# Optimization experiments

Measured on AMD Instinct MI355X. Metric: run time of the kernel, lower is better.

## Reference

```python
import jax, jax.numpy as jnp
import numpy as np

B, C, H, W = 8, 256, 64, 64
GROUPS = 8
EPS = 1e-5


def setup_inputs() -> dict:
    key = jax.random.key(0)
    ks = jax.random.split(key, 10)
    s = 1.0 / np.sqrt(C)
    return {
        "x": jax.random.normal(ks[0], (B, C, H, W), dtype=jnp.float32),
        "gn_gamma": jnp.ones((C,), jnp.float32),
        "gn_beta": jnp.zeros((C,), jnp.float32),
        "wq": jax.random.uniform(ks[1], (C, C), jnp.float32, -s, s),
        "bq": jax.random.uniform(ks[2], (C,), jnp.float32, -s, s),
        "wk": jax.random.uniform(ks[3], (C, C), jnp.float32, -s, s),
        "bk": jax.random.uniform(ks[4], (C,), jnp.float32, -s, s),
        "wv": jax.random.uniform(ks[5], (C, C), jnp.float32, -s, s),
        "bv": jax.random.uniform(ks[6], (C,), jnp.float32, -s, s),
        "wp": jax.random.uniform(ks[7], (C, C), jnp.float32, -s, s),
        "bp": jax.random.uniform(ks[8], (C,), jnp.float32, -s, s),
    }


def _group_norm(x, gamma, beta):
    b, c, h, w = x.shape
    xg = x.reshape(b, GROUPS, c // GROUPS, h, w)
    mu = jnp.mean(xg, axis=(2, 3, 4), keepdims=True)
    var = jnp.mean(jnp.square(xg - mu), axis=(2, 3, 4), keepdims=True)
    xn = ((xg - mu) * jax.lax.rsqrt(var + EPS)).reshape(b, c, h, w)
    return xn * gamma[None, :, None, None] + beta[None, :, None, None]


def reference(x, gn_gamma, gn_beta, wq, bq, wk, bk, wv, bv, wp, bp):
    b, c, h, w = x.shape
    xn = _group_norm(x, gn_gamma, gn_beta)
    xf = xn.reshape(b, c, h * w)  # [b, c, n]
    # 1x1 Conv1d == per-position channel matmul
    q = jnp.einsum('oc,bcn->bon', wq, xf) + bq[None, :, None]
    k = jnp.einsum('oc,bcn->bon', wk, xf) + bk[None, :, None]
    v = jnp.einsum('oc,bcn->bon', wv, xf) + bv[None, :, None]
    scale = 1.0 / jnp.sqrt(jnp.asarray(c, xf.dtype))
    # attn[b,i,j] = softmax_j(q[:,i]^T k[:,j] / sqrt(c))
    attn = jax.nn.softmax(jnp.einsum('bci,bcj->bij', q, k) * scale, axis=-1)
    # out[b,c,i] = sum_j v[b,c,j] * attn[b,i,j]
    out = jnp.einsum('bcj,bij->bci', v, attn)
    out = jnp.einsum('oc,bcn->bon', wp, out) + bp[None, :, None]
    return x + out.reshape(b, c, h, w)
```

## Files before the change

### kernel.cpp

```cpp
#include <hip/hip_runtime.h>


typedef __bf16 bf16x8 __attribute__((ext_vector_type(8)));
typedef __bf16 bf16x4 __attribute__((ext_vector_type(4)));
typedef float floatx4 __attribute__((ext_vector_type(4)));
typedef float floatx16 __attribute__((ext_vector_type(16)));

constexpr int Bb = 8, Cc_ = 256, HW = 4096;
constexpr int BNT = Bb * HW;

__device__ __forceinline__ void load_lds16(const void* g, void* l) {
  __builtin_amdgcn_global_load_lds((const __attribute__((address_space(1))) void*)g,
                                   (__attribute__((address_space(3))) void*)l, 16, 0, 0);
}

#define MEMFENCE asm volatile("" ::: "memory")
__device__ __forceinline__ void bar_sync() {
  MEMFENCE;
  __builtin_amdgcn_s_barrier();
  MEMFENCE;
}

__global__ __launch_bounds__(256) void gn_part(const float* __restrict__ x,
                                               float* __restrict__ part) {
  int sub = blockIdx.x & 7;
  int bg = blockIdx.x >> 3;
  const float4* p = (const float4*)(x + (size_t)bg * 131072 + (size_t)sub * 16384);
  int tid = threadIdx.x;
  float s = 0.f, ss = 0.f;
#pragma unroll
  for (int i = 0; i < 16; ++i) {
    float4 v = p[i * 256 + tid];
    s += v.x + v.y + v.z + v.w;
    ss += v.x * v.x + v.y * v.y + v.z * v.z + v.w * v.w;
  }
  for (int off = 32; off; off >>= 1) { s += __shfl_down(s, off); ss += __shfl_down(ss, off); }
  __shared__ float red[8];
  int wv = tid >> 6, ln = tid & 63;
  if (ln == 0) { red[wv] = s; red[4 + wv] = ss; }
  __syncthreads();
  if (tid == 0) {
    part[blockIdx.x * 2] = red[0] + red[1] + red[2] + red[3];
    part[blockIdx.x * 2 + 1] = red[4] + red[5] + red[6] + red[7];
  }
}

__global__ __launch_bounds__(256) void gn_norm_t(const float* __restrict__ x,
                                                 const float* __restrict__ part,
                                                 const float* __restrict__ gamma,
                                                 const float* __restrict__ beta,
                                                 __bf16* __restrict__ Xt) {
  __shared__ float tile[64][65];
  __shared__ float sst[4];
  int b = blockIdx.z, c0 = blockIdx.y * 64, n0 = blockIdx.x * 64;
  int tid = threadIdx.x;
  if (tid < 2) {
    int g = b * 8 + (c0 >> 5) + tid;
    float s = 0.f, ss = 0.f;
#pragma unroll
    for (int k = 0; k < 8; ++k) { s += part[(g * 8 + k) * 2]; ss += part[(g * 8 + k) * 2 + 1]; }
    float mean = s / 131072.f;
    float var = ss / 131072.f - mean * mean;
    sst[tid * 2] = mean;
    sst[tid * 2 + 1] = rsqrtf(var + 1e-5f);
  }
  int cl = tid >> 4, nl = (tid & 15) * 4;
  const float* xb = x + ((size_t)b * Cc_ + c0) * HW + n0;
#pragma unroll
  for (int i = 0; i < 4; ++i) {
    int c = cl + i * 16;
    float4 v = *(const float4*)&xb[(size_t)c * HW + nl];
    tile[c][nl] = v.x; tile[c][nl + 1] = v.y; tile[c][nl + 2] = v.z; tile[c][nl + 3] = v.w;
  }
  __syncthreads();
#pragma unroll
  for (int i = 0; i < 16; ++i) {
    int idx = i * 256 + tid;
    int n = idx >> 6, c = idx & 63;
    int gc = c0 + c;
    float mean = sst[(c >> 5) * 2], rstd = sst[(c >> 5) * 2 + 1];
    float v = (tile[c][n] - mean) * rstd * gamma[gc] + beta[gc];
    Xt[((size_t)b * HW + n0 + n) * Cc_ + gc] = (__bf16)v;
  }
}

__global__ __launch_bounds__(256) void pack_w(const float* __restrict__ wq, const float* __restrict__ wk,
                                              const float* __restrict__ wv, const float* __restrict__ wp,
                                              const float* __restrict__ bq, const float* __restrict__ bk,
                                              const float* __restrict__ bv, const float* __restrict__ bp,
                                              __bf16* __restrict__ Wqk, __bf16* __restrict__ Wv,
                                              __bf16* __restrict__ Wp, float* __restrict__ Bqk,
                                              float* __restrict__ Bv, float* __restrict__ Bp) {
  int i = blockIdx.x * 256 + threadIdx.x;
  if (i < 65536) {
    Wqk[i] = (__bf16)wq[i];
    Wqk[65536 + i] = (__bf16)wk[i];
    Wv[i] = (__bf16)wv[i];
    Wp[i] = (__bf16)wp[i];
  }
  if (i < 256) { Bqk[i] = bq[i]; Bqk[256 + i] = bk[i]; Bv[i] = bv[i]; Bp[i] = bp[i]; }
}

template <int BM, int BN, int WM, int WN, int EPI>
__global__ __launch_bounds__(256) void gemm_bt(
    const __bf16* __restrict__ A, int lda,
    const __bf16* __restrict__ B, int ldb,
    __bf16* __restrict__ C, int ldc,
    int K, float scale,
    const float* __restrict__ bias,
    const float* __restrict__ resid,
    float* __restrict__ outF) {
  constexpr int TM = WM / 16, TN = WN / 16;
  __shared__ __bf16 As[BM * 32];
  __shared__ __bf16 Bs[BN * 32];

  const int tid = threadIdx.x;
  const int wave = tid >> 6, lane = tid & 63;
  const int wr = wave >> 1, wc = wave & 1;
  const int quad = lane >> 4, l16 = lane & 15;
  const int m0 = blockIdx.y * BM, n0 = blockIdx.x * BN;
  const int srow = lane >> 2;
  const int scol = (lane & 3) * 8;

  floatx4 acc[TM][TN] = {};

  const int kTiles = K / 32;
  for (int kt = 0; kt < kTiles; ++kt) {
    const int k0 = kt * 32;
    __syncthreads();
#pragma unroll
    for (int i = 0; i < BM / 64; ++i) {
      int row = i * 64 + wave * 16 + srow;
      load_lds16(A + (size_t)(m0 + row) * lda + k0 + scol, &As[(i * 64 + wave * 16) * 32]);
    }
#pragma unroll
    for (int i = 0; i < BN / 64; ++i) {
      int row = i * 64 + wave * 16 + srow;
      load_lds16(B + (size_t)(n0 + row) * ldb + k0 + scol, &Bs[(i * 64 + wave * 16) * 32]);
    }
    __syncthreads();

    bf16x8 af[TM], bfr[TN];
#pragma unroll
    for (int i = 0; i < TM; ++i)
      af[i] = *(const bf16x8*)&As[(wr * WM + i * 16 + l16) * 32 + quad * 8];
#pragma unroll
    for (int j = 0; j < TN; ++j)
      bfr[j] = *(const bf16x8*)&Bs[(wc * WN + j * 16 + l16) * 32 + quad * 8];
#pragma unroll
    for (int i = 0; i < TM; ++i)
#pragma unroll
      for (int j = 0; j < TN; ++j)
        acc[i][j] = __builtin_amdgcn_mfma_f32_16x16x32_bf16(af[i], bfr[j], acc[i][j], 0, 0, 0);
  }

#pragma unroll
  for (int i = 0; i < TM; ++i) {
#pragma unroll
    for (int j = 0; j < TN; ++j) {
      int gc = n0 + wc * WN + j * 16 + l16;
#pragma unroll
      for (int r = 0; r < 4; ++r) {
        int gr = m0 + wr * WM + i * 16 + quad * 4 + r;
        float v = acc[i][j][r] * scale;
        if constexpr (EPI == 1) v += bias[gc];
        if constexpr (EPI == 2) v += bias[gr];
        if constexpr (EPI == 3) {
          int bb = gc >> 12, nn = gc & 4095;
          size_t oidx = (size_t)bb * (Cc_ * HW) + (size_t)gr * HW + nn;
          outF[oidx] = v + bias[gr] + resid[oidx];
        } else {
          C[(size_t)gr * ldc + gc] = (__bf16)v;
        }
      }
    }
  }
}

__global__ __launch_bounds__(256, 2) void flash_attn(const __bf16* __restrict__ QK,
                                                     const __bf16* __restrict__ V,
                                                     __bf16* __restrict__ O) {
  __shared__ __align__(16) __bf16 smem[36864];
  __shared__ float Lb[2][64];
  __shared__ __align__(16) float Linv[64];
  __bf16* Ks = smem;
  __bf16* Vt = smem + 16384;
  __bf16* Pb = smem + 32768;

  const int tid = threadIdx.x;
  const int w = tid >> 6, lane = tid & 63;
  const int r = w & 1, h = w >> 1;
  const int l31 = lane & 31, hh = lane >> 5;
  const int b = blockIdx.x & 7;
  const int m0 = (blockIdx.x >> 3) * 64;
  const int q = 32 * r + l31;

  bf16x8 qf[16];
  {
    const size_t qrow = (size_t)(b * HW + m0 + q);
#pragma unroll
    for (int kc = 0; kc < 16; ++kc) {
      qf[kc] = *(const bf16x8*)&QK[qrow * 512 + kc * 16 + hh * 8];
#pragma unroll
      for (int e = 0; e < 8; ++e) qf[kc][e] = (__bf16)((float)qf[kc][e] * 0.0625f);
    }
  }

  floatx16 oacc[4] = {};
  float l_run = 0.f;

  const int ks_slot = lane & 31, ks_rin = lane >> 5;
  const int vt_slot = lane & 7, vt_rin = lane >> 3;

#pragma unroll
  for (int i = 0; i < 8; ++i) {
    int rl = w * 16 + i * 2 + ks_rin;
    load_lds16(QK + (size_t)(b * HW + rl) * 512 + 256 + ((ks_slot ^ (rl & 31)) << 3),
               &Ks[(w * 16 + i * 2) * 256]);
  }

  for (int jt = 0; jt < 64; ++jt) {
    const int j0 = jt * 64;
    asm volatile("s_waitcnt lgkmcnt(0)" ::: "memory");
    bar_sync();
#pragma unroll
    for (int i = 0; i < 8; ++i) {
      int cl = w * 64 + i * 8 + vt_rin;
      load_lds16(V + (size_t)cl * BNT + (b * HW + j0 + ((vt_slot ^ (cl & 7)) << 3)),
                 &Vt[(w * 64 + i * 8) * 64]);
    }
    asm volatile("s_waitcnt vmcnt(8)" ::: "memory");
    bar_sync();

    floatx16 sacc = {};
    {
      const int jl = 32 * h + l31;
      const __bf16* krow = &Ks[jl * 256];
      const int jx = jl & 31;
      __builtin_amdgcn_s_setprio(1);
#pragma unroll
      for (int kc = 0; kc < 16; ++kc) {
        bf16x8 kfv = *(const bf16x8*)&krow[((kc * 2 + hh) ^ jx) << 3];
        sacc = __builtin_amdgcn_mfma_f32_32x32x16_bf16(kfv, qf[kc], sacc, 0, 0, 0);
      }
      __builtin_amdgcn_s_setprio(0);
    }

    float ls = 0.f;
#pragma unroll
    for (int i = 0; i < 16; ++i) {
      float p = __expf(sacc[i]);
      sacc[i] = p;
      ls += p;
    }
    l_run += ls;
#pragma unroll
    for (int g = 0; g < 4; ++g) {
      bf16x4 pk;
#pragma unroll
      for (int k = 0; k < 4; ++k) pk[k] = (__bf16)sacc[g * 4 + k];
      *(bf16x4*)&Pb[q * 64 + ((((4 * h + g) ^ (l31 & 7)) << 3) + 4 * hh)] = pk;
    }

    asm volatile("s_waitcnt vmcnt(0) lgkmcnt(0)" ::: "memory");
    bar_sync();

    if (jt < 63) {
#pragma unroll
      for (int i = 0; i < 8; ++i) {
        int rl = w * 16 + i * 2 + ks_rin;
        load_lds16(QK + (size_t)(b * HW + j0 + 64 + rl) * 512 + 256 + ((ks_slot ^ (rl & 31)) << 3),
                   &Ks[(w * 16 + i * 2) * 256]);
      }
    }

    __builtin_amdgcn_s_setprio(1);
#pragma unroll
    for (int ks = 0; ks < 4; ++ks) {
      bf16x8 pf = *(const bf16x8*)&Pb[q * 64 + (((ks * 2 + hh) ^ (l31 & 7)) << 3)];
#pragma unroll
      for (int nt = 0; nt < 4; ++nt) {
        int cl = h * 128 + nt * 32 + l31;
        bf16x8 vf = *(const bf16x8*)&Vt[cl * 64 + (((ks * 2 + hh) ^ (cl & 7)) << 3)];
        oacc[nt] = __builtin_amdgcn_mfma_f32_32x32x16_bf16(pf, vf, oacc[nt], 0, 0, 0);
      }
    }
    __builtin_amdgcn_s_setprio(0);
  }

  __syncthreads();
  float l2 = l_run + __shfl_xor(l_run, 32);
  if (hh == 0) Lb[h][q] = l2;
  __syncthreads();
  if (tid < 64) Linv[tid] = 1.f / (Lb[0][tid] + Lb[1][tid]);
  __syncthreads();
  __bf16* Os = smem;
#pragma unroll
  for (int g = 0; g < 4; ++g) {
    floatx4 lv = *(const floatx4*)&Linv[32 * r + g * 8 + 4 * hh];
#pragma unroll
    for (int k = 0; k < 4; ++k) {
      int qloc = 32 * r + g * 8 + 4 * hh + k;
#pragma unroll
      for (int nt = 0; nt < 4; ++nt) {
        int c = h * 128 + nt * 32 + l31;
        Os[qloc * 256 + c] = (__bf16)(oacc[nt][g * 4 + k] * lv[k]);
      }
    }
  }
  __syncthreads();
  const float4* src = (const float4*)Os;
  float4* dst = (float4*)(O + (size_t)(b * HW + m0) * 256);
#pragma unroll
  for (int i = 0; i < 8; ++i) dst[i * 256 + tid] = src[i * 256 + tid];
}

extern "C" void kernel_launch(void* const* d_in, const int* in_sizes, int n_in,
                              void* d_out, int out_size, void* d_ws, size_t ws_size,
                              hipStream_t stream) {
  const float* x = (const float*)d_in[0];
  const float* gamma = (const float*)d_in[1];
  const float* beta = (const float*)d_in[2];
  const float* wq = (const float*)d_in[3];
  const float* bq = (const float*)d_in[4];
  const float* wk = (const float*)d_in[5];
  const float* bk = (const float*)d_in[6];
  const float* wv = (const float*)d_in[7];
  const float* bv = (const float*)d_in[8];
  const float* wp = (const float*)d_in[9];
  const float* bp = (const float*)d_in[10];
  float* out = (float*)d_out;

  char* ws = (char*)d_ws;
  size_t off = 0;
  auto alloc = [&](size_t n) { size_t o = off; off = (off + n + 255) & ~(size_t)255; return o; };
  __bf16* XT = (__bf16*)(ws + alloc((size_t)BNT * Cc_ * 2));
  __bf16* QK = (__bf16*)(ws + alloc((size_t)BNT * 512 * 2));
  __bf16* V  = (__bf16*)(ws + alloc((size_t)Cc_ * BNT * 2));
  __bf16* O  = (__bf16*)(ws + alloc((size_t)BNT * Cc_ * 2));
  __bf16* WQK = (__bf16*)(ws + alloc(512 * 256 * 2));
  __bf16* WV  = (__bf16*)(ws + alloc(256 * 256 * 2));
  __bf16* WP  = (__bf16*)(ws + alloc(256 * 256 * 2));
  float* BQK = (float*)(ws + alloc(512 * 4));
  float* BV  = (float*)(ws + alloc(256 * 4));
  float* BP  = (float*)(ws + alloc(256 * 4));
  float* PART = (float*)(ws + alloc(512 * 2 * 4));

  pack_w<<<dim3(256), dim3(256), 0, stream>>>(wq, wk, wv, wp, bq, bk, bv, bp,
                                              WQK, WV, WP, BQK, BV, BP);
  gn_part<<<dim3(512), dim3(256), 0, stream>>>(x, PART);
  gn_norm_t<<<dim3(64, 4, 8), dim3(256), 0, stream>>>(x, PART, gamma, beta, XT);

  gemm_bt<128, 128, 64, 64, 1><<<dim3(512 / 128, BNT / 128), dim3(256), 0, stream>>>(
      XT, 256, WQK, 256, QK, 512, 256, 1.0f, BQK, nullptr, nullptr);
  gemm_bt<128, 128, 64, 64, 2><<<dim3(BNT / 128, 256 / 128), dim3(256), 0, stream>>>(
      WV, 256, XT, 256, V, BNT, 256, 1.0f, BV, nullptr, nullptr);

  flash_attn<<<dim3(512), dim3(256), 0, stream>>>(QK, V, O);

  gemm_bt<128, 128, 64, 64, 3><<<dim3(BNT / 128, 256 / 128), dim3(256), 0, stream>>>(
      WP, 256, O, 256, nullptr, 0, 256, 1.0f, BP, x, out);
}
```

Measured before the change: 317.8 us.

## Prefetch K tiles into registers and double-buffer V in LDS in flash attention

Flash attention now loads K tiles straight from global memory into per-wave registers and issues the load for the next tile right after the score MFMAs, instead of staging K through shared memory. V tiles are double-buffered in shared memory, and the next tile is fetched while the current one is consumed. This cuts the barriers per iteration from three to two and lets global loads overlap with compute. In exchange it uses about 64 more VGPRs per thread, and waves that share the same h re-fetch the same K rows from global or L2 rather than sharing one LDS copy.

```diff
diff --git a/kernel.cpp b/kernel.cpp
--- a/kernel.cpp
+++ b/kernel.cpp
@@ -183,8 +183,6 @@
   __shared__ __align__(16) __bf16 smem[36864];
   __shared__ float Lb[2][64];
   __shared__ __align__(16) float Linv[64];
-  __bf16* Ks = smem;
-  __bf16* Vt = smem + 16384;
   __bf16* Pb = smem + 32768;
 
   const int tid = threadIdx.x;
@@ -206,44 +204,38 @@
     }
   }
 
+  const __bf16* kbase = QK + (size_t)(b * HW + 32 * h + l31) * 512 + 256 + hh * 8;
+  bf16x8 kf[16];
+#pragma unroll
+  for (int kc = 0; kc < 16; ++kc) kf[kc] = *(const bf16x8*)&kbase[kc * 16];
+
+  const int vt_slot = lane & 7, vt_rin = lane >> 3;
+#pragma unroll
+  for (int i = 0; i < 8; ++i) {
+    int cl = w * 64 + i * 8 + vt_rin;
+    load_lds16(V + (size_t)cl * BNT + (b * HW + ((vt_slot ^ (cl & 7)) << 3)),
+               &smem[(w * 64 + i * 8) * 64]);
+  }
+
   floatx16 oacc[4] = {};
   float l_run = 0.f;
 
-  const int ks_slot = lane & 31, ks_rin = lane >> 5;
-  const int vt_slot = lane & 7, vt_rin = lane >> 3;
-
-#pragma unroll
-  for (int i = 0; i < 8; ++i) {
-    int rl = w * 16 + i * 2 + ks_rin;
-    load_lds16(QK + (size_t)(b * HW + rl) * 512 + 256 + ((ks_slot ^ (rl & 31)) << 3),
-               &Ks[(w * 16 + i * 2) * 256]);
-  }
-
   for (int jt = 0; jt < 64; ++jt) {
     const int j0 = jt * 64;
-    asm volatile("s_waitcnt lgkmcnt(0)" ::: "memory");
-    bar_sync();
-#pragma unroll
-    for (int i = 0; i < 8; ++i) {
-      int cl = w * 64 + i * 8 + vt_rin;
-      load_lds16(V + (size_t)cl * BNT + (b * HW + j0 + ((vt_slot ^ (cl & 7)) << 3)),
-                 &Vt[(w * 64 + i * 8) * 64]);
-    }
-    asm volatile("s_waitcnt vmcnt(8)" ::: "memory");
-    bar_sync();
+    __bf16* Vc = smem + ((jt & 1) << 14);
+    __bf16* Vn = smem + (((jt + 1) & 1) << 14);
 
     floatx16 sacc = {};
-    {
-      const int jl = 32 * h + l31;
-      const __bf16* krow = &Ks[jl * 256];
-      const int jx = jl & 31;
-      __builtin_amdgcn_s_setprio(1);
-#pragma unroll
-      for (int kc = 0; kc < 16; ++kc) {
-        bf16x8 kfv = *(const bf16x8*)&krow[((kc * 2 + hh) ^ jx) << 3];
-        sacc = __builtin_amdgcn_mfma_f32_32x32x16_bf16(kfv, qf[kc], sacc, 0, 0, 0);
-      }
-      __builtin_amdgcn_s_setprio(0);
+    __builtin_amdgcn_s_setprio(1);
+#pragma unroll
+    for (int kc = 0; kc < 16; ++kc)
+      sacc = __builtin_amdgcn_mfma_f32_32x32x16_bf16(kf[kc], qf[kc], sacc, 0, 0, 0);
+    __builtin_amdgcn_s_setprio(0);
+
+    if (jt < 63) {
+      const __bf16* kb = kbase + (size_t)(j0 + 64) * 512;
+#pragma unroll
+      for (int kc = 0; kc < 16; ++kc) kf[kc] = *(const bf16x8*)&kb[kc * 16];
     }
 
     float ls = 0.f;
@@ -254,6 +246,9 @@
       ls += p;
     }
     l_run += ls;
+
+    asm volatile("s_waitcnt lgkmcnt(0)" ::: "memory");
+    bar_sync();
 #pragma unroll
     for (int g = 0; g < 4; ++g) {
       bf16x4 pk;
@@ -261,18 +256,18 @@
       for (int k = 0; k < 4; ++k) pk[k] = (__bf16)sacc[g * 4 + k];
       *(bf16x4*)&Pb[q * 64 + ((((4 * h + g) ^ (l31 & 7)) << 3) + 4 * hh)] = pk;
     }
-
-    asm volatile("s_waitcnt vmcnt(0) lgkmcnt(0)" ::: "memory");
+    if (jt < 63) {
+#pragma unroll
+      for (int i = 0; i < 8; ++i) {
+        int cl = w * 64 + i * 8 + vt_rin;
+        load_lds16(V + (size_t)cl * BNT + (b * HW + j0 + 64 + ((vt_slot ^ (cl & 7)) << 3)),
+                   &Vn[(w * 64 + i * 8) * 64]);
+      }
+      asm volatile("s_waitcnt vmcnt(24) lgkmcnt(0)" ::: "memory");
+    } else {
+      asm volatile("s_waitcnt vmcnt(0) lgkmcnt(0)" ::: "memory");
+    }
     bar_sync();
-
-    if (jt < 63) {
-#pragma unroll
-      for (int i = 0; i < 8; ++i) {
-        int rl = w * 16 + i * 2 + ks_rin;
-        load_lds16(QK + (size_t)(b * HW + j0 + 64 + rl) * 512 + 256 + ((ks_slot ^ (rl & 31)) << 3),
-                   &Ks[(w * 16 + i * 2) * 256]);
-      }
-    }
 
     __builtin_amdgcn_s_setprio(1);
 #pragma unroll
@@ -281,7 +276,7 @@
 #pragma unroll
       for (int nt = 0; nt < 4; ++nt) {
         int cl = h * 128 + nt * 32 + l31;
-        bf16x8 vf = *(const bf16x8*)&Vt[cl * 64 + (((ks * 2 + hh) ^ (cl & 7)) << 3)];
+        bf16x8 vf = *(const bf16x8*)&Vc[cl * 64 + (((ks * 2 + hh) ^ (cl & 7)) << 3)];
         oacc[nt] = __builtin_amdgcn_mfma_f32_32x32x16_bf16(pf, vf, oacc[nt], 0, 0, 0);
       }
     }
```

Measured after the change: 471.5 us. +48.4%, slower.

## Warp-specialize flash attention into QK-softmax and PV producer/consumer waves

Applied to the files above, without the earlier changes.

Splits the four waves of the attention block into two roles. Two waves compute QK^T scores and exp for all 64 queries and write P into a double-buffered LDS tile. The other two waves load V and accumulate P·V for the previous tile, so the two matmul stages run one tile apart and overlap. This removes one of the per-tile barriers and lets K and V loads proceed independently. In exchange it doubles per-wave accumulator and Q-fragment registers, which may hurt occupancy under launch_bounds(256,2), and it depends on barrier counts matching exactly between the two branches.

```diff
diff --git a/kernel.cpp b/kernel.cpp
--- a/kernel.cpp
+++ b/kernel.cpp
@@ -180,136 +180,184 @@
 __global__ __launch_bounds__(256, 2) void flash_attn(const __bf16* __restrict__ QK,
                                                      const __bf16* __restrict__ V,
                                                      __bf16* __restrict__ O) {
-  __shared__ __align__(16) __bf16 smem[36864];
-  __shared__ float Lb[2][64];
-  __shared__ __align__(16) float Linv[64];
+  __shared__ __align__(16) __bf16 smem[40960];
   __bf16* Ks = smem;
   __bf16* Vt = smem + 16384;
   __bf16* Pb = smem + 32768;
 
   const int tid = threadIdx.x;
   const int w = tid >> 6, lane = tid & 63;
-  const int r = w & 1, h = w >> 1;
   const int l31 = lane & 31, hh = lane >> 5;
   const int b = blockIdx.x & 7;
   const int m0 = (blockIdx.x >> 3) * 64;
-  const int q = 32 * r + l31;
-
-  bf16x8 qf[16];
-  {
-    const size_t qrow = (size_t)(b * HW + m0 + q);
-#pragma unroll
-    for (int kc = 0; kc < 16; ++kc) {
-      qf[kc] = *(const bf16x8*)&QK[qrow * 512 + kc * 16 + hh * 8];
-#pragma unroll
-      for (int e = 0; e < 8; ++e) qf[kc][e] = (__bf16)((float)qf[kc][e] * 0.0625f);
-    }
-  }
-
-  floatx16 oacc[4] = {};
-  float l_run = 0.f;
-
-  const int ks_slot = lane & 31, ks_rin = lane >> 5;
-  const int vt_slot = lane & 7, vt_rin = lane >> 3;
-
-#pragma unroll
-  for (int i = 0; i < 8; ++i) {
-    int rl = w * 16 + i * 2 + ks_rin;
-    load_lds16(QK + (size_t)(b * HW + rl) * 512 + 256 + ((ks_slot ^ (rl & 31)) << 3),
-               &Ks[(w * 16 + i * 2) * 256]);
-  }
-
-  for (int jt = 0; jt < 64; ++jt) {
-    const int j0 = jt * 64;
-    asm volatile("s_waitcnt lgkmcnt(0)" ::: "memory");
-    bar_sync();
-#pragma unroll
-    for (int i = 0; i < 8; ++i) {
-      int cl = w * 64 + i * 8 + vt_rin;
-      load_lds16(V + (size_t)cl * BNT + (b * HW + j0 + ((vt_slot ^ (cl & 7)) << 3)),
-                 &Vt[(w * 64 + i * 8) * 64]);
-    }
-    asm volatile("s_waitcnt vmcnt(8)" ::: "memory");
-    bar_sync();
-
-    floatx16 sacc = {};
-    {
-      const int jl = 32 * h + l31;
-      const __bf16* krow = &Ks[jl * 256];
-      const int jx = jl & 31;
+
+  if (w < 2) {
+    const int h = w;
+    const int ks_slot = lane & 31, ks_rin = lane >> 5;
+
+    bf16x8 qf[2][16];
+#pragma unroll
+    for (int qt = 0; qt < 2; ++qt) {
+      const size_t qrow = (size_t)(b * HW + m0 + qt * 32 + l31);
+#pragma unroll
+      for (int kc = 0; kc < 16; ++kc) {
+        qf[qt][kc] = *(const bf16x8*)&QK[qrow * 512 + kc * 16 + hh * 8];
+#pragma unroll
+        for (int e = 0; e < 8; ++e) qf[qt][kc][e] = (__bf16)((float)qf[qt][kc][e] * 0.0625f);
+      }
+    }
+#pragma unroll
+    for (int i = 0; i < 16; ++i) {
+      int rl = h * 32 + i * 2 + ks_rin;
+      load_lds16(QK + (size_t)(b * HW + rl) * 512 + 256 + ((ks_slot ^ (rl & 31)) << 3),
+                 &Ks[(h * 32 + i * 2) * 256]);
+    }
+    bar_sync();
+
+    float lr0 = 0.f, lr1 = 0.f;
+    const int jl = h * 32 + l31;
+    const __bf16* krow = &Ks[jl * 256];
+    const int jx = l31;
+
+    for (int t = 0; t < 64; ++t) {
+      asm volatile("s_waitcnt vmcnt(0)" ::: "memory");
+      floatx16 s0 = {}, s1 = {};
       __builtin_amdgcn_s_setprio(1);
 #pragma unroll
       for (int kc = 0; kc < 16; ++kc) {
         bf16x8 kfv = *(const bf16x8*)&krow[((kc * 2 + hh) ^ jx) << 3];
-        sacc = __builtin_amdgcn_mfma_f32_32x32x16_bf16(kfv, qf[kc], sacc, 0, 0, 0);
+        s0 = __builtin_amdgcn_mfma_f32_32x32x16_bf16(kfv, qf[0][kc], s0, 0, 0, 0);
+        s1 = __builtin_amdgcn_mfma_f32_32x32x16_bf16(kfv, qf[1][kc], s1, 0, 0, 0);
       }
       __builtin_amdgcn_s_setprio(0);
-    }
-
-    float ls = 0.f;
+      asm volatile("s_waitcnt lgkmcnt(0)" ::: "memory");
+      if (t < 63) {
+#pragma unroll
+        for (int i = 0; i < 16; ++i) {
+          int rl = h * 32 + i * 2 + ks_rin;
+          load_lds16(QK + (size_t)(b * HW + (t + 1) * 64 + rl) * 512 + 256 +
+                         ((ks_slot ^ (rl & 31)) << 3),
+                     &Ks[(h * 32 + i * 2) * 256]);
+        }
+      }
+      float ls0 = 0.f, ls1 = 0.f;
+#pragma unroll
+      for (int i = 0; i < 16; ++i) {
+        float p0 = __expf(s0[i]); s0[i] = p0; ls0 += p0;
+        float p1 = __expf(s1[i]); s1[i] = p1; ls1 += p1;
+      }
+      lr0 += ls0; lr1 += ls1;
+      __bf16* Pt = Pb + ((t & 1) << 12);
+#pragma unroll
+      for (int g = 0; g < 4; ++g) {
+        bf16x4 pk0, pk1;
+#pragma unroll
+        for (int k = 0; k < 4; ++k) { pk0[k] = (__bf16)s0[g * 4 + k]; pk1[k] = (__bf16)s1[g * 4 + k]; }
+        *(bf16x4*)&Pt[(l31) * 64 + ((((4 * h + g) ^ (l31 & 7)) << 3) + 4 * hh)] = pk0;
+        *(bf16x4*)&Pt[(32 + l31) * 64 + ((((4 * h + g) ^ (l31 & 7)) << 3) + 4 * hh)] = pk1;
+      }
+      asm volatile("s_waitcnt lgkmcnt(0)" ::: "memory");
+      bar_sync();
+    }
+
+    float* Lb = (float*)(smem + 32768);
+    float l20 = lr0 + __shfl_xor(lr0, 32);
+    float l21 = lr1 + __shfl_xor(lr1, 32);
+    if (hh == 0) { Lb[h * 64 + l31] = l20; Lb[h * 64 + 32 + l31] = l21; }
+    asm volatile("s_waitcnt lgkmcnt(0)" ::: "memory");
+    bar_sync();
+    if (w == 0) Lb[128 + lane] = 1.f / (Lb[lane] + Lb[64 + lane]);
+    asm volatile("s_waitcnt lgkmcnt(0)" ::: "memory");
+    bar_sync();
+    bar_sync();
+  } else {
+    const int ch = w - 2;
+    const int vt_slot = lane & 7, vt_rin = lane >> 3;
+
 #pragma unroll
     for (int i = 0; i < 16; ++i) {
-      float p = __expf(sacc[i]);
-      sacc[i] = p;
-      ls += p;
-    }
-    l_run += ls;
-#pragma unroll
-    for (int g = 0; g < 4; ++g) {
-      bf16x4 pk;
-#pragma unroll
-      for (int k = 0; k < 4; ++k) pk[k] = (__bf16)sacc[g * 4 + k];
-      *(bf16x4*)&Pb[q * 64 + ((((4 * h + g) ^ (l31 & 7)) << 3) + 4 * hh)] = pk;
-    }
-
-    asm volatile("s_waitcnt vmcnt(0) lgkmcnt(0)" ::: "memory");
-    bar_sync();
-
-    if (jt < 63) {
-#pragma unroll
-      for (int i = 0; i < 8; ++i) {
-        int rl = w * 16 + i * 2 + ks_rin;
-        load_lds16(QK + (size_t)(b * HW + j0 + 64 + rl) * 512 + 256 + ((ks_slot ^ (rl & 31)) << 3),
-                   &Ks[(w * 16 + i * 2) * 256]);
-      }
-    }
-
-    __builtin_amdgcn_s_setprio(1);
-#pragma unroll
-    for (int ks = 0; ks < 4; ++ks) {
-      bf16x8 pf = *(const bf16x8*)&Pb[q * 64 + (((ks * 2 + hh) ^ (l31 & 7)) << 3)];
-#pragma unroll
-      for (int nt = 0; nt < 4; ++nt) {
-        int cl = h * 128 + nt * 32 + l31;
-        bf16x8 vf = *(const bf16x8*)&Vt[cl * 64 + (((ks * 2 + hh) ^ (cl & 7)) << 3)];
-        oacc[nt] = __builtin_amdgcn_mfma_f32_32x32x16_bf16(pf, vf, oacc[nt], 0, 0, 0);
-      }
-    }
-    __builtin_amdgcn_s_setprio(0);
-  }
-
-  __syncthreads();
-  float l2 = l_run + __shfl_xor(l_run, 32);
-  if (hh == 0) Lb[h][q] = l2;
-  __syncthreads();
-  if (tid < 64) Linv[tid] = 1.f / (Lb[0][tid] + Lb[1][tid]);
-  __syncthreads();
-  __bf16* Os = smem;
-#pragma unroll
-  for (int g = 0; g < 4; ++g) {
-    floatx4 lv = *(const floatx4*)&Linv[32 * r + g * 8 + 4 * hh];
-#pragma unroll
-    for (int k = 0; k < 4; ++k) {
-      int qloc = 32 * r + g * 8 + 4 * hh + k;
-#pragma unroll
-      for (int nt = 0; nt < 4; ++nt) {
-        int c = h * 128 + nt * 32 + l31;
-        Os[qloc * 256 + c] = (__bf16)(oacc[nt][g * 4 + k] * lv[k]);
-      }
-    }
-  }
-  __syncthreads();
-  const float4* src = (const float4*)Os;
+      int cl = ch * 128 + i * 8 + vt_rin;
+      load_lds16(V + (size_t)cl * BNT + (b * HW + ((vt_slot ^ (cl & 7)) << 3)),
+                 &Vt[(ch * 128 + i * 8) * 64]);
+    }
+    bar_sync();
+
+    floatx16 oacc[2][4] = {};
+
+    for (int t = 0; t < 64; ++t) {
+      asm volatile("s_waitcnt vmcnt(0)" ::: "memory");
+      if (t > 0) {
+        const __bf16* Pp = Pb + (((t - 1) & 1) << 12);
+        __builtin_amdgcn_s_setprio(1);
+#pragma unroll
+        for (int ks = 0; ks < 4; ++ks) {
+          bf16x8 pf0 = *(const bf16x8*)&Pp[(l31) * 64 + (((ks * 2 + hh) ^ (l31 & 7)) << 3)];
+          bf16x8 pf1 = *(const bf16x8*)&Pp[(32 + l31) * 64 + (((ks * 2 + hh) ^ (l31 & 7)) << 3)];
+#pragma unroll
+          for (int nt = 0; nt < 4; ++nt) {
+            int cl = ch * 128 + nt * 32 + l31;
+            bf16x8 vf = *(const bf16x8*)&Vt[cl * 64 + (((ks * 2 + hh) ^ (cl & 7)) << 3)];
+            oacc[0][nt] = __builtin_amdgcn_mfma_f32_32x32x16_bf16(pf0, vf, oacc[0][nt], 0, 0, 0);
+            oacc[1][nt] = __builtin_amdgcn_mfma_f32_32x32x16_bf16(pf1, vf, oacc[1][nt], 0, 0, 0);
+          }
+        }
+        __builtin_amdgcn_s_setprio(0);
+        asm volatile("s_waitcnt lgkmcnt(0)" ::: "memory");
+#pragma unroll
+        for (int i = 0; i < 16; ++i) {
+          int cl = ch * 128 + i * 8 + vt_rin;
+          load_lds16(V + (size_t)cl * BNT + (b * HW + t * 64 + ((vt_slot ^ (cl & 7)) << 3)),
+                     &Vt[(ch * 128 + i * 8) * 64]);
+        }
+      }
+      bar_sync();
+    }
+
+    asm volatile("s_waitcnt vmcnt(0)" ::: "memory");
+    {
+      const __bf16* Pp = Pb + 4096;
+      __builtin_amdgcn_s_setprio(1);
+#pragma unroll
+      for (int ks = 0; ks < 4; ++ks) {
+        bf16x8 pf0 = *(const bf16x8*)&Pp[(l31) * 64 + (((ks * 2 + hh) ^ (l31 & 7)) << 3)];
+        bf16x8 pf1 = *(const bf16x8*)&Pp[(32 + l31) * 64 + (((ks * 2 + hh) ^ (l31 & 7)) << 3)];
+#pragma unroll
+        for (int nt = 0; nt < 4; ++nt) {
+          int cl = ch * 128 + nt * 32 + l31;
+          bf16x8 vf = *(const bf16x8*)&Vt[cl * 64 + (((ks * 2 + hh) ^ (cl & 7)) << 3)];
+          oacc[0][nt] = __builtin_amdgcn_mfma_f32_32x32x16_bf16(pf0, vf, oacc[0][nt], 0, 0, 0);
+          oacc[1][nt] = __builtin_amdgcn_mfma_f32_32x32x16_bf16(pf1, vf, oacc[1][nt], 0, 0, 0);
+        }
+      }
+      __builtin_amdgcn_s_setprio(0);
+    }
+    asm volatile("s_waitcnt lgkmcnt(0)" ::: "memory");
+    bar_sync();
+    bar_sync();
+
+    const float* Linv = (const float*)(smem + 32768) + 128;
+    __bf16* Os = smem;
+#pragma unroll
+    for (int qt = 0; qt < 2; ++qt) {
+#pragma unroll
+      for (int g = 0; g < 4; ++g) {
+        floatx4 lv = *(const floatx4*)&Linv[qt * 32 + g * 8 + 4 * hh];
+#pragma unroll
+        for (int k = 0; k < 4; ++k) {
+          int qloc = qt * 32 + g * 8 + 4 * hh + k;
+#pragma unroll
+          for (int nt = 0; nt < 4; ++nt) {
+            int c = ch * 128 + nt * 32 + l31;
+            Os[qloc * 256 + c] = (__bf16)(oacc[qt][nt][g * 4 + k] * lv[k]);
+          }
+        }
+      }
+    }
+    asm volatile("s_waitcnt lgkmcnt(0)" ::: "memory");
+    bar_sync();
+  }
+
+  const float4* src = (const float4*)smem;
   float4* dst = (float4*)(O + (size_t)(b * HW + m0) * 256);
 #pragma unroll
   for (int i = 0; i < 8; ++i) dst[i * 256 + tid] = src[i * 256 + tid];
```

New measurement: 316.4 us. About the same (-0.4%).
